# Kernel optimization log

Hardware: AMD Instinct MI355X
Metric: run time of the kernel (lower is better)

## Reference

```python
import jax, jax.numpy as jnp
import numpy as np

B, T, D, H = 8, 256, 1024, 512
NUM_SPANS = T * (T + 1) // 2          # triangular span enumeration
K = int(2.0 * T)                      # pruning_ratio * num_tokens
NUM_GOLD = 10
NEG = -1e20                           # allennlp replace_masked_values fill

# static triangular (start, end) index tables: for start in range(T): for end in range(start, T)
_starts = np.repeat(np.arange(T), np.arange(T, 0, -1))
_ends = np.concatenate([np.arange(s, T) for s in range(T)])
START_IDX = jnp.asarray(_starts, dtype=jnp.int32)
END_IDX = jnp.asarray(_ends, dtype=jnp.int32)


def setup_inputs() -> dict:
    key = jax.random.key(0)
    ks = jax.random.split(key, 8)
    inputs = jax.random.normal(ks[0], (B, T, D), dtype=jnp.float32)
    input_mask = jnp.ones((B, T), dtype=jnp.int32)
    # gold spans with start <= end, all in range (sorted along last dim)
    answer_spans = jnp.sort(jax.random.randint(ks[1], (B, NUM_GOLD, 2), 0, T), axis=-1)
    sD = 1.0 / np.sqrt(D)
    sH = 1.0 / np.sqrt(H)
    W_start = jax.random.uniform(ks[2], (D, H), jnp.float32, -sD, sD)
    b_start = jax.random.uniform(ks[3], (H,), jnp.float32, -sD, sD)
    W_end = jax.random.uniform(ks[4], (D, H), jnp.float32, -sD, sD)
    b_end = jax.random.uniform(ks[5], (H,), jnp.float32, -sD, sD)
    w_score = jax.random.uniform(ks[6], (H, 1), jnp.float32, -sH, sH)
    b_score = jax.random.uniform(ks[7], (1,), jnp.float32, -sH, sH)
    return {"inputs": inputs, "input_mask": input_mask, "answer_spans": answer_spans,
            "W_start": W_start, "b_start": b_start, "W_end": W_end, "b_end": b_end,
            "w_score": w_score, "b_score": b_score}


def reference(inputs, input_mask, answer_spans, W_start, b_start, W_end, b_end, w_score, b_score):
    # SpanRepAssembly: project starts/ends, pairwise-sum over triangular spans
    hs = inputs @ W_start + b_start                        # [B,T,H]
    he = inputs @ W_end + b_end                            # [B,T,H]
    span_hidden = hs[:, START_IDX, :] + he[:, END_IDX, :]  # [B,S,H]
    m = input_mask.astype(bool)
    span_mask = m[:, START_IDX] & m[:, END_IDX]            # [B,S]

    # span scorer: ReLU -> Linear(H,1)
    scores = jax.nn.relu(span_hidden) @ w_score + b_score  # [B,S,1]
    scores = jnp.where(span_mask[..., None], scores, NEG)

    # Pruner: top-k by score, indices sorted ascending, gather
    _, top_idx = jax.lax.top_k(scores[..., 0], K)          # [B,K]
    top_idx = jnp.sort(top_idx, axis=1)
    top_logits = jnp.take_along_axis(scores, top_idx[..., None], axis=1)       # [B,K,1]
    top_mask = jnp.take_along_axis(span_mask, top_idx, axis=1)[..., None].astype(jnp.float32)
    top_probs = jax.nn.sigmoid(top_logits) * top_mask

    # gold prediction map (union policy): labels[b, tri_index(span)] = 1
    s0 = answer_spans[..., 0].astype(jnp.int32)
    e0 = answer_spans[..., 1].astype(jnp.int32)
    gmask = (s0 >= 0)
    arg_idx = (2 * s0 * T - s0 * s0 + s0) // 2 + (e0 - s0)
    arg_idx = jnp.where(gmask, arg_idx, 0)
    labels = jnp.zeros((B, NUM_SPANS), jnp.float32)
    labels = labels.at[jnp.arange(B)[:, None], arg_idx].max(gmask.astype(jnp.float32))
    pred = jnp.take_along_axis(labels[..., None], top_idx[..., None], axis=1)  # [B,K,1]

    # BCE-with-logits, weight=top_mask, reduction='sum' (stable form)
    l = top_logits
    bce = jnp.maximum(l, 0.0) - l * pred + jnp.log1p(jnp.exp(-jnp.abs(l)))
    loss = jnp.sum(top_mask * bce)
    return top_probs, loss
```

## Files before the change

### kernel.cpp

```cpp
#include <hip/hip_runtime.h>
#include <hip/hip_bf16.h>
#include <math.h>

#define BB 8
#define TT 256
#define DD 1024
#define HH 512
#define NSPANS 32896
#define KK 512
#define NEGV -1e20f
#define NCH 32
#define CHSZ 1028
#define NT32 36

typedef __attribute__((ext_vector_type(8))) short bf16x8;
typedef __attribute__((ext_vector_type(4))) float f32x4;

__device__ inline unsigned short f2bf(float f) {
    unsigned u = __float_as_uint(f);
    return (unsigned short)((u + 0x7FFFu + ((u >> 16) & 1u)) >> 16);
}
__device__ inline float bf2f(unsigned short u) {
    return __uint_as_float(((unsigned)u) << 16);
}
__device__ inline void split3(float v, unsigned short& a, unsigned short& b,
                              unsigned short& c) {
    a = f2bf(v);           float r  = v - bf2f(a);
    b = f2bf(r);           float r2 = r - bf2f(b);
    c = f2bf(r2);
}

__global__ __launch_bounds__(256) void prep(
    const float* __restrict__ X,
    const float* __restrict__ Ws, const float* __restrict__ We,
    unsigned short* __restrict__ x0, unsigned short* __restrict__ x1,
    unsigned short* __restrict__ x2, unsigned short* __restrict__ wt,
    unsigned* __restrict__ zp)
{
    const int blk = blockIdx.x;
    const int tid = threadIdx.x;

    if (blk < 2048) {
        const int i4 = blk * 256 + tid;
        const float4 v = ((const float4*)X)[i4];
        const float vv[4] = {v.x, v.y, v.z, v.w};
        ushort4 h0, h1, h2;
        unsigned short* p0 = (unsigned short*)&h0;
        unsigned short* p1 = (unsigned short*)&h1;
        unsigned short* p2 = (unsigned short*)&h2;
        #pragma unroll
        for (int j = 0; j < 4; ++j) split3(vv[j], p0[j], p1[j], p2[j]);
        ((ushort4*)x0)[i4] = h0;
        ((ushort4*)x1)[i4] = h1;
        ((ushort4*)x2)[i4] = h2;
    } else if (blk < 3072) {
        __shared__ float lt[32][33];
        const int blk2 = blk - 2048;
        const int z   = blk2 >> 9;
        const int rem = blk2 & 511;
        const int k0  = (rem >> 4) * 32;
        const int h0  = (rem & 15) * 32;

        const float* Wz = z ? We : Ws;
        {
            const int row = tid >> 3, c4 = tid & 7;
            const float4 v = *(const float4*)&Wz[(k0 + row) * HH + h0 + c4 * 4];
            lt[row][c4*4 + 0] = v.x;
            lt[row][c4*4 + 1] = v.y;
            lt[row][c4*4 + 2] = v.z;
            lt[row][c4*4 + 3] = v.w;
        }
        __syncthreads();
        {
            const int n = h0 + (tid >> 3), kq = tid & 7;
            ushort4 o0, o1, o2;
            unsigned short* q0 = (unsigned short*)&o0;
            unsigned short* q1 = (unsigned short*)&o1;
            unsigned short* q2 = (unsigned short*)&o2;
            #pragma unroll
            for (int u = 0; u < 4; ++u)
                split3(lt[kq*4 + u][tid >> 3], q0[u], q1[u], q2[u]);
            unsigned short* base = wt + (size_t)z * 3 * 524288;
            const int off = n * 1024 + k0 + kq * 4;
            *(ushort4*)&base[0 * 524288 + off] = o0;
            *(ushort4*)&base[1 * 524288 + off] = o1;
            *(ushort4*)&base[2 * 524288 + off] = o2;
        }
    } else {
        const int i = (blk - 3072) * 256 + tid;
        for (int k = i; k < 32777; k += 32 * 256) zp[k] = 0u;
    }
}

__global__ __launch_bounds__(256) void gemm_mfma(
    const unsigned short* __restrict__ xs,
    const unsigned short* __restrict__ wt,
    const float* __restrict__ bs, const float* __restrict__ be,
    float* __restrict__ hs, float* __restrict__ he)
{
    const int bid = blockIdx.x;
    const int lg  = ((bid & 7) << 6) + (bid >> 3);
    const int z   = lg >> 8;
    const int my  = (lg & 255) >> 3, nx = lg & 7;
    const int m0 = my * 64, n0 = nx * 64;

    const unsigned short* __restrict__ W = wt + (size_t)z * 3 * 524288;
    const float* __restrict__ bias = z ? be : bs;
    float* __restrict__ Y = z ? he : hs;

    __shared__ __align__(16) unsigned short la[3][64][72];
    __shared__ __align__(16) unsigned short lb[3][64][72];

    const int tid = threadIdx.x;
    const int wave = tid >> 6, lane = tid & 63;
    const int wm = (wave >> 1) * 32, wn = (wave & 1) * 32;

    f32x4 acc[2][2];
    #pragma unroll
    for (int i = 0; i < 2; ++i)
        #pragma unroll
        for (int j = 0; j < 2; ++j) acc[i][j] = (f32x4){0.f, 0.f, 0.f, 0.f};

    const int rA = lane & 15;
    const int kq = lane >> 4;

    for (int kt = 0; kt < 16; ++kt) {
        const int k0 = kt * 64;
        __syncthreads();
        #pragma unroll
        for (int sp = 0; sp < 3; ++sp) {
            #pragma unroll
            for (int it = 0; it < 2; ++it) {
                const int idx = it * 256 + tid;
                const int row = idx >> 3, c8 = idx & 7;
                *(int4*)&la[sp][row][c8 * 8] =
                    *(const int4*)&xs[(size_t)sp * 2097152 + (m0 + row) * 1024 + k0 + c8 * 8];
                *(int4*)&lb[sp][row][c8 * 8] =
                    *(const int4*)&W[(size_t)sp * 524288 + (n0 + row) * 1024 + k0 + c8 * 8];
            }
        }
        __syncthreads();

        #pragma unroll
        for (int s = 0; s < 2; ++s) {
            const int kl = s * 32 + kq * 8;
            bf16x8 af[3][2], bg[3][2];
            #pragma unroll
            for (int sp = 0; sp < 3; ++sp) {
                #pragma unroll
                for (int f = 0; f < 2; ++f) {
                    af[sp][f] = *(const bf16x8*)&la[sp][wm + f * 16 + rA][kl];
                    bg[sp][f] = *(const bf16x8*)&lb[sp][wn + f * 16 + rA][kl];
                }
            }
            #pragma unroll
            for (int fm = 0; fm < 2; ++fm)
                #pragma unroll
                for (int fn = 0; fn < 2; ++fn) {
                    acc[fm][fn] = __builtin_amdgcn_mfma_f32_16x16x32_bf16(
                        af[0][fm], bg[0][fn], acc[fm][fn], 0, 0, 0);
                    acc[fm][fn] = __builtin_amdgcn_mfma_f32_16x16x32_bf16(
                        af[0][fm], bg[1][fn], acc[fm][fn], 0, 0, 0);
                    acc[fm][fn] = __builtin_amdgcn_mfma_f32_16x16x32_bf16(
                        af[1][fm], bg[0][fn], acc[fm][fn], 0, 0, 0);
                    acc[fm][fn] = __builtin_amdgcn_mfma_f32_16x16x32_bf16(
                        af[1][fm], bg[1][fn], acc[fm][fn], 0, 0, 0);
                    acc[fm][fn] = __builtin_amdgcn_mfma_f32_16x16x32_bf16(
                        af[0][fm], bg[2][fn], acc[fm][fn], 0, 0, 0);
                    acc[fm][fn] = __builtin_amdgcn_mfma_f32_16x16x32_bf16(
                        af[2][fm], bg[0][fn], acc[fm][fn], 0, 0, 0);
                }
        }
    }

    const int col = lane & 15, rq = lane >> 4;
    #pragma unroll
    for (int fm = 0; fm < 2; ++fm)
        #pragma unroll
        for (int fn = 0; fn < 2; ++fn) {
            const int nn = n0 + wn + fn * 16 + col;
            const float bv = bias[nn];
            #pragma unroll
            for (int r = 0; r < 4; ++r) {
                const int mm = m0 + wm + fm * 16 + rq * 4 + r;
                Y[mm * HH + nn] = acc[fm][fn][r] + bv;
            }
        }
}

__device__ inline unsigned f2key(float f) {
    unsigned u = __float_as_uint(f);
    return u ^ ((u & 0x80000000u) ? 0xFFFFFFFFu : 0x80000000u);
}

__global__ __launch_bounds__(256) void span_scores(
    const float* __restrict__ hs, const float* __restrict__ he,
    const float* __restrict__ w_score, const float* __restrict__ b_score,
    const int* __restrict__ input_mask, float* __restrict__ scores,
    unsigned* __restrict__ hist12)
{
    const int bx = blockIdx.x;
    const int b = bx / NT32;
    int tI = bx - b * NT32;
    int i = 0, cum = 0;
    while (tI >= cum + (8 - i)) { cum += 8 - i; ++i; }
    const int j = i + (tI - cum);
    const int s0 = i * 32, e0 = j * 32;

    __shared__ __align__(16) float shs[32][132];
    __shared__ __align__(16) float she[32][132];
    __shared__ __align__(16) float swc[128];
    __shared__ unsigned lh[2048];

    const int tid = threadIdx.x;
    const float4* hs4 = (const float4*)hs;
    const float4* he4 = (const float4*)he;

    for (int idx = tid; idx < 2048; idx += 256) lh[idx] = 0;

    const int ii = tid >> 4, jj = tid & 15;

    float4 acc[2][2];
    #pragma unroll
    for (int p = 0; p < 2; ++p)
        #pragma unroll
        for (int q = 0; q < 2; ++q) acc[p][q] = make_float4(0.f, 0.f, 0.f, 0.f);

    for (int ck = 0; ck < 4; ++ck) {
        const int kc = ck * 128;
        __syncthreads();
        #pragma unroll
        for (int l = 0; l < 4; ++l) {
            const int idx = l * 256 + tid;
            const int row = idx >> 5, c4 = idx & 31;
            *(float4*)&shs[row][c4 * 4] =
                hs4[((b*TT + s0 + row) * HH + kc) / 4 + c4];
            *(float4*)&she[row][c4 * 4] =
                he4[((b*TT + e0 + row) * HH + kc) / 4 + c4];
        }
        if (tid < 32) *(float4*)&swc[tid * 4] =
            ((const float4*)w_score)[kc / 4 + tid];
        __syncthreads();

        #pragma unroll 4
        for (int c4 = 0; c4 < 32; ++c4) {
            const float4 w  = *(const float4*)&swc[c4 * 4];
            const float4 a0 = *(const float4*)&shs[ii][c4 * 4];
            const float4 a1 = *(const float4*)&shs[ii + 16][c4 * 4];
            const float4 v0 = *(const float4*)&she[jj][c4 * 4];
            const float4 v1 = *(const float4*)&she[jj + 16][c4 * 4];
            #pragma unroll
            for (int p = 0; p < 2; ++p) {
                const float4 a = p ? a1 : a0;
                #pragma unroll
                for (int q = 0; q < 2; ++q) {
                    const float4 v = q ? v1 : v0;
                    acc[p][q].x += fmaxf(a.x + v.x, 0.f) * w.x;
                    acc[p][q].y += fmaxf(a.y + v.y, 0.f) * w.y;
                    acc[p][q].z += fmaxf(a.z + v.z, 0.f) * w.z;
                    acc[p][q].w += fmaxf(a.w + v.w, 0.f) * w.w;
                }
            }
        }
    }

    const float bsc = b_score[0];
    #pragma unroll
    for (int p = 0; p < 2; ++p) {
        const int s = s0 + ii + p * 16;
        #pragma unroll
        for (int q = 0; q < 2; ++q) {
            const int e = e0 + jj + q * 16;
            if (e >= s) {
                const float4 a4 = acc[p][q];
                float scv = (a4.x + a4.y) + (a4.z + a4.w) + bsc;
                if (!(input_mask[b*TT + s] && input_mask[b*TT + e])) scv = NEGV;
                scores[b*NSPANS + s*TT - (s*(s-1))/2 + (e - s)] = scv;
                const unsigned bin = f2key(scv) >> 20;
                atomicAdd(&lh[bin >> 1], 1u << ((bin & 1u) * 16));
            }
        }
    }
    __syncthreads();

    for (int idx = tid; idx < 2048; idx += 256) {
        const unsigned w = lh[idx];
        const unsigned lo = w & 0xFFFFu, hi = w >> 16;
        if (lo) atomicAdd(&hist12[b*4096 + 2*idx],     lo);
        if (hi) atomicAdd(&hist12[b*4096 + 2*idx + 1], hi);
    }
}

__global__ __launch_bounds__(256) void findcompact(
    const float* __restrict__ scores, const unsigned* __restrict__ hist12,
    unsigned* __restrict__ thrInfo,
    unsigned* __restrict__ cand, unsigned* __restrict__ candCnt)
{
    const int b = blockIdx.x >> 5, ch = blockIdx.x & 31;
    const unsigned* h = hist12 + b * 4096;
    const int tid = threadIdx.x;
    const int lane = tid & 63, wave = tid >> 6;

    const int topbin = 4095 - tid * 16;
    unsigned psum = 0;
    #pragma unroll
    for (int j = 0; j < 16; ++j) psum += h[topbin - j];

    unsigned inc = psum;
    #pragma unroll
    for (int off = 1; off < 64; off <<= 1) {
        unsigned v = __shfl_up(inc, off);
        if (lane >= off) inc += v;
    }
    __shared__ unsigned wsum4[4], wpre4[4];
    __shared__ unsigned shp[2];
    if (lane == 63) wsum4[wave] = inc;
    __syncthreads();
    if (tid == 0) { unsigned c = 0; for (int w = 0; w < 4; ++w) { wpre4[w] = c; c += wsum4[w]; } }
    __syncthreads();

    const unsigned before = wpre4[wave] + inc - psum;
    if (before < KK && before + psum >= KK) {
        unsigned cum = before;
        int bin = topbin;
        #pragma unroll
        for (int j = 0; j < 16; ++j) {
            const unsigned c = h[topbin - j];
            if (cum + c >= KK) { bin = topbin - j; break; }
            cum += c;
        }
        shp[0] = (unsigned)bin;
        shp[1] = KK - cum;
        thrInfo[b*4 + 0] = (unsigned)bin;
        thrInfo[b*4 + 1] = KK - cum;
    }
    __syncthreads();
    const unsigned p12 = shp[0];

    const float* sc = scores + b * NSPANS;
    const int base = ch * CHSZ;
    for (int i = base + tid; i < base + CHSZ; i += 256) {
        const unsigned key = f2key(sc[i]);
        if ((key >> 20) == p12) {
            const unsigned pos = atomicAdd(&candCnt[b], 1u);
            cand[b*NSPANS + pos] = key & 0xFFFFFu;
        }
    }
}

__global__ __launch_bounds__(1024) void refine(
    const unsigned* __restrict__ cand, const unsigned* __restrict__ candCnt,
    const float* __restrict__ scores,
    unsigned* __restrict__ thrInfo, unsigned* __restrict__ chunkBase)
{
    const int b = blockIdx.x;
    const unsigned* cd = cand + b*NSPANS;
    const unsigned n = candCnt[b];
    const unsigned remaining = thrInfo[b*4 + 1];
    const int tid = threadIdx.x;
    const int lane = tid & 63, wave = tid >> 6;

    __shared__ unsigned hist[1024];
    __shared__ unsigned wsum[16], wpre[16];
    __shared__ unsigned sh[2], shT[2];

    hist[tid] = 0;
    __syncthreads();
    for (unsigned i = tid; i < n; i += 1024) atomicAdd(&hist[(cd[i] >> 10) & 1023u], 1u);
    __syncthreads();
    {
        const unsigned psum = hist[1023 - tid];
        unsigned inc = psum;
        #pragma unroll
        for (int off = 1; off < 64; off <<= 1) {
            unsigned v = __shfl_up(inc, off);
            if (lane >= off) inc += v;
        }
        if (lane == 63) wsum[wave] = inc;
        __syncthreads();
        if (tid == 0) { unsigned c = 0; for (int w = 0; w < 16; ++w) { wpre[w] = c; c += wsum[w]; } }
        __syncthreads();
        const unsigned before = wpre[wave] + inc - psum;
        if (before < remaining && before + psum >= remaining && psum > 0) {
            sh[0] = 1023u - (unsigned)tid;
            sh[1] = remaining - before;
        }
        __syncthreads();
    }
    const unsigned b1 = sh[0], rem1 = sh[1];
    __syncthreads();

    hist[tid] = 0;
    __syncthreads();
    for (unsigned i = tid; i < n; i += 1024) {
        const unsigned v = cd[i];
        if (((v >> 10) & 1023u) == b1) atomicAdd(&hist[v & 1023u], 1u);
    }
    __syncthreads();
    {
        const unsigned psum = hist[1023 - tid];
        unsigned inc = psum;
        #pragma unroll
        for (int off = 1; off < 64; off <<= 1) {
            unsigned v = __shfl_up(inc, off);
            if (lane >= off) inc += v;
        }
        if (lane == 63) wsum[wave] = inc;
        __syncthreads();
        if (tid == 0) { unsigned c = 0; for (int w = 0; w < 16; ++w) { wpre[w] = c; c += wsum[w]; } }
        __syncthreads();
        const unsigned before = wpre[wave] + inc - psum;
        if (before < rem1 && before + psum >= rem1 && psum > 0) {
            const unsigned thrv = (thrInfo[b*4 + 0] << 20) | (b1 << 10) | (1023u - (unsigned)tid);
            thrInfo[b*4 + 2] = thrv;
            thrInfo[b*4 + 3] = rem1 - before;
            shT[0] = thrv;
            shT[1] = rem1 - before;
        }
    }
    __syncthreads();
    const unsigned thr = shT[0], ties = shT[1];

    __shared__ unsigned cg[NCH], ce[NCH];
    const float* sc = scores + b*NSPANS;
    #pragma unroll
    for (int q = 0; q < 2; ++q) {
        const int ch = wave*2 + q;
        const int base = ch*CHSZ, end = base + CHSZ;
        unsigned g = 0, e = 0;
        for (int i = base + lane; i < end; i += 64) {
            const unsigned key = f2key(sc[i]);
            g += (key > thr); e += (key == thr);
        }
        #pragma unroll
        for (int off = 32; off; off >>= 1) { g += __shfl_down(g, off); e += __shfl_down(e, off); }
        if (lane == 0) { cg[ch] = g; ce[ch] = e; }
    }
    __syncthreads();

    if (tid == 0) {
        unsigned out = 0, eqp = 0;
        for (int c = 0; c < NCH; ++c) {
            chunkBase[(b*NCH + c)*2 + 0] = out;
            chunkBase[(b*NCH + c)*2 + 1] = eqp;
            const unsigned room = (eqp >= ties) ? 0u : (ties - eqp);
            const unsigned taken = (ce[c] < room) ? ce[c] : room;
            out += cg[c] + taken;
            eqp += ce[c];
        }
    }
}

__global__ __launch_bounds__(256) void scatter_final(
    const float* __restrict__ scores, const unsigned* __restrict__ thrInfo,
    const unsigned* __restrict__ chunkBase, const int* __restrict__ answer_spans,
    float* __restrict__ chunkLoss, unsigned* __restrict__ ticket,
    float* __restrict__ out)
{
    const int b = blockIdx.x >> 5, ch = blockIdx.x & 31;
    const float* sc = scores + b*NSPANS;
    const unsigned thr = thrInfo[b*4 + 2], ties = thrInfo[b*4 + 3];
    unsigned outPos = chunkBase[(b*NCH + ch)*2 + 0];
    unsigned eqPos  = chunkBase[(b*NCH + ch)*2 + 1];

    const int tid = threadIdx.x, wave = tid >> 6, lane = tid & 63;
    const unsigned long long lmask = (1ull << lane) - 1ull;
    __shared__ unsigned wS[4], wE[4];
    __shared__ int gold[10];
    __shared__ float wLoss[4];
    __shared__ unsigned lastFlag;

    if (tid < 10) {
        const int s0 = answer_spans[b*20 + tid*2];
        const int e0 = answer_spans[b*20 + tid*2 + 1];
        gold[tid] = (s0 >= 0) ? ((2*s0*TT - s0*s0 + s0)/2 + (e0 - s0)) : -1;
    }
    __syncthreads();

    float lsum = 0.f;
    const int base = ch*CHSZ;
    for (int seg = base; seg < base + CHSZ; seg += 256) {
        const int i = seg + tid;
        const bool valid = (i < base + CHSZ);
        const float v = valid ? sc[i] : 0.f;
        const unsigned key = valid ? f2key(v) : 0u;
        const bool g  = valid && key > thr;
        const bool eq = valid && key == thr;

        const unsigned long long meq = __ballot(eq);
        if (lane == 0) wE[wave] = (unsigned)__popcll(meq);
        __syncthreads();

        unsigned eqPre = eqPos;
        for (int w = 0; w < wave; ++w) eqPre += wE[w];
        const unsigned myEqRank = eqPre + (unsigned)__popcll(meq & lmask);
        const bool sel = g || (eq && myEqRank < ties);

        const unsigned long long msel = __ballot(sel);
        if (lane == 0) wS[wave] = (unsigned)__popcll(msel);
        __syncthreads();

        unsigned selPre = outPos;
        for (int w = 0; w < wave; ++w) selPre += wS[w];
        if (sel) {
            const unsigned pos = b*KK + selPre + (unsigned)__popcll(msel & lmask);
            float prob = 0.f;
            if (v > -1e19f) {
                prob = 1.f / (1.f + expf(-v));
                float pred = 0.f;
                #pragma unroll
                for (int gq = 0; gq < 10; ++gq)
                    if (gold[gq] == i) pred = 1.f;
                lsum += fmaxf(v, 0.f) - v*pred + log1pf(expf(-fabsf(v)));
            }
            out[pos] = prob;
        }

        unsigned totS = 0, totE = 0;
        #pragma unroll
        for (int w = 0; w < 4; ++w) { totS += wS[w]; totE += wE[w]; }
        __syncthreads();
        outPos += totS; eqPos += totE;
    }

    #pragma unroll
    for (int off = 32; off; off >>= 1) lsum += __shfl_down(lsum, off);
    if (lane == 0) wLoss[wave] = lsum;
    __syncthreads();
    if (tid == 0) {
        chunkLoss[b*NCH + ch] = (wLoss[0] + wLoss[1]) + (wLoss[2] + wLoss[3]);
        __threadfence();
        lastFlag = atomicAdd(ticket, 1u);
    }
    __syncthreads();

    if (lastFlag == BB*NCH - 1) {
        __threadfence();
        float cl = atomicAdd(&chunkLoss[tid], 0.f);
        #pragma unroll
        for (int off = 32; off; off >>= 1) cl += __shfl_down(cl, off);
        if (lane == 0) wLoss[wave] = cl;
        __syncthreads();
        if (tid == 0)
            out[BB*KK] = (wLoss[0] + wLoss[1]) + (wLoss[2] + wLoss[3]);
    }
}

extern "C" void kernel_launch(void* const* d_in, const int* in_sizes, int n_in,
                              void* d_out, int out_size, void* d_ws, size_t ws_size,
                              hipStream_t stream)
{
    const float* inputs       = (const float*)d_in[0];
    const int*   input_mask   = (const int*)  d_in[1];
    const int*   answer_spans = (const int*)  d_in[2];
    const float* W_start      = (const float*)d_in[3];
    const float* b_start      = (const float*)d_in[4];
    const float* W_end        = (const float*)d_in[5];
    const float* b_end        = (const float*)d_in[6];
    const float* w_score      = (const float*)d_in[7];
    const float* b_score      = (const float*)d_in[8];
    float* out = (float*)d_out;
    unsigned* ws = (unsigned*)d_ws;

    float*    hs       = (float*)(ws);
    float*    he       = (float*)(ws + 1048576);
    float*    scores   = (float*)(ws + 2097152);
    unsigned* thrInfo  = ws + 2364416;
    unsigned* chunkBase= ws + 2364448;
    unsigned* hist12   = ws + 2364960;
    unsigned* candCnt  = ws + 2397728;
    unsigned* ticket   = ws + 2397736;
    unsigned short* xs = (unsigned short*)(ws + 2397740);
    unsigned short* wt = (unsigned short*)(ws + 5543468);
    float*    chunkLoss= (float*)(ws + 7116332);
    unsigned* cand     = (unsigned*)hs;

    prep<<<3104, 256, 0, stream>>>(inputs, W_start, W_end,
                                   xs, xs + 2097152, xs + 4194304, wt, hist12);

    gemm_mfma<<<512, 256, 0, stream>>>(xs, wt, b_start, b_end, hs, he);

    span_scores<<<BB*NT32, 256, 0, stream>>>(hs, he, w_score, b_score, input_mask,
                                             scores, hist12);

    findcompact  <<<BB*NCH, 256, 0, stream>>>(scores, hist12, thrInfo, cand, candCnt);
    refine       <<<BB, 1024, 0, stream>>>(cand, candCnt, scores, thrInfo, chunkBase);
    scatter_final<<<BB*NCH, 256, 0, stream>>>(scores, thrInfo, chunkBase,
                                              answer_spans, chunkLoss, ticket, out);
}
```

Baseline: 111.8 us.

## Fuse candidate compaction and threshold refinement via last-block ticket

```diff
diff --git a/kernel.cpp b/kernel.cpp
--- a/kernel.cpp
+++ b/kernel.cpp
@@ -88,7 +88,7 @@
         }
     } else {
         const int i = (blk - 3072) * 256 + tid;
-        for (int k = i; k < 32777; k += 32 * 256) zp[k] = 0u;
+        for (int k = i; k < 32785; k += 32 * 256) zp[k] = 0u;
     }
 }
 
@@ -291,142 +291,168 @@
     }
 }
 
-__global__ __launch_bounds__(256) void findcompact(
+__global__ __launch_bounds__(256) void findcompact_refine(
     const float* __restrict__ scores, const unsigned* __restrict__ hist12,
     unsigned* __restrict__ thrInfo,
-    unsigned* __restrict__ cand, unsigned* __restrict__ candCnt)
+    unsigned* __restrict__ cand, unsigned* __restrict__ candCnt,
+    unsigned* __restrict__ ticket2, unsigned* __restrict__ chunkBase)
 {
     const int b = blockIdx.x >> 5, ch = blockIdx.x & 31;
     const unsigned* h = hist12 + b * 4096;
     const int tid = threadIdx.x;
     const int lane = tid & 63, wave = tid >> 6;
 
-    const int topbin = 4095 - tid * 16;
-    unsigned psum = 0;
-    #pragma unroll
-    for (int j = 0; j < 16; ++j) psum += h[topbin - j];
-
-    unsigned inc = psum;
-    #pragma unroll
-    for (int off = 1; off < 64; off <<= 1) {
-        unsigned v = __shfl_up(inc, off);
-        if (lane >= off) inc += v;
-    }
     __shared__ unsigned wsum4[4], wpre4[4];
     __shared__ unsigned shp[2];
-    if (lane == 63) wsum4[wave] = inc;
-    __syncthreads();
-    if (tid == 0) { unsigned c = 0; for (int w = 0; w < 4; ++w) { wpre4[w] = c; c += wsum4[w]; } }
-    __syncthreads();
-
-    const unsigned before = wpre4[wave] + inc - psum;
-    if (before < KK && before + psum >= KK) {
-        unsigned cum = before;
-        int bin = topbin;
-        #pragma unroll
-        for (int j = 0; j < 16; ++j) {
-            const unsigned c = h[topbin - j];
-            if (cum + c >= KK) { bin = topbin - j; break; }
-            cum += c;
-        }
-        shp[0] = (unsigned)bin;
-        shp[1] = KK - cum;
-        thrInfo[b*4 + 0] = (unsigned)bin;
-        thrInfo[b*4 + 1] = KK - cum;
-    }
-    __syncthreads();
-    const unsigned p12 = shp[0];
-
-    const float* sc = scores + b * NSPANS;
-    const int base = ch * CHSZ;
-    for (int i = base + tid; i < base + CHSZ; i += 256) {
-        const unsigned key = f2key(sc[i]);
-        if ((key >> 20) == p12) {
-            const unsigned pos = atomicAdd(&candCnt[b], 1u);
-            cand[b*NSPANS + pos] = key & 0xFFFFFu;
-        }
-    }
-}
-
-__global__ __launch_bounds__(1024) void refine(
-    const unsigned* __restrict__ cand, const unsigned* __restrict__ candCnt,
-    const float* __restrict__ scores,
-    unsigned* __restrict__ thrInfo, unsigned* __restrict__ chunkBase)
-{
-    const int b = blockIdx.x;
-    const unsigned* cd = cand + b*NSPANS;
-    const unsigned n = candCnt[b];
-    const unsigned remaining = thrInfo[b*4 + 1];
-    const int tid = threadIdx.x;
-    const int lane = tid & 63, wave = tid >> 6;
-
+    __shared__ unsigned myTicket;
     __shared__ unsigned hist[1024];
-    __shared__ unsigned wsum[16], wpre[16];
-    __shared__ unsigned sh[2], shT[2];
-
-    hist[tid] = 0;
-    __syncthreads();
-    for (unsigned i = tid; i < n; i += 1024) atomicAdd(&hist[(cd[i] >> 10) & 1023u], 1u);
-    __syncthreads();
+    __shared__ unsigned shR[2];
+    __shared__ unsigned cg[NCH], ce[NCH];
+
     {
-        const unsigned psum = hist[1023 - tid];
+        const int topbin = 4095 - tid * 16;
+        unsigned psum = 0;
+        #pragma unroll
+        for (int j = 0; j < 16; ++j) psum += h[topbin - j];
+
         unsigned inc = psum;
         #pragma unroll
         for (int off = 1; off < 64; off <<= 1) {
             unsigned v = __shfl_up(inc, off);
             if (lane >= off) inc += v;
         }
-        if (lane == 63) wsum[wave] = inc;
-        __syncthreads();
-        if (tid == 0) { unsigned c = 0; for (int w = 0; w < 16; ++w) { wpre[w] = c; c += wsum[w]; } }
-        __syncthreads();
-        const unsigned before = wpre[wave] + inc - psum;
-        if (before < remaining && before + psum >= remaining && psum > 0) {
-            sh[0] = 1023u - (unsigned)tid;
-            sh[1] = remaining - before;
-        }
-        __syncthreads();
-    }
-    const unsigned b1 = sh[0], rem1 = sh[1];
-    __syncthreads();
-
-    hist[tid] = 0;
-    __syncthreads();
-    for (unsigned i = tid; i < n; i += 1024) {
-        const unsigned v = cd[i];
-        if (((v >> 10) & 1023u) == b1) atomicAdd(&hist[v & 1023u], 1u);
-    }
-    __syncthreads();
+        if (lane == 63) wsum4[wave] = inc;
+        __syncthreads();
+        if (tid == 0) { unsigned c = 0; for (int w = 0; w < 4; ++w) { wpre4[w] = c; c += wsum4[w]; } }
+        __syncthreads();
+
+        const unsigned before = wpre4[wave] + inc - psum;
+        if (before < KK && before + psum >= KK) {
+            unsigned cum = before;
+            int bin = topbin;
+            #pragma unroll
+            for (int j = 0; j < 16; ++j) {
+                const unsigned c = h[topbin - j];
+                if (cum + c >= KK) { bin = topbin - j; break; }
+                cum += c;
+            }
+            shp[0] = (unsigned)bin;
+            shp[1] = KK - cum;
+            thrInfo[b*4 + 0] = (unsigned)bin;
+            thrInfo[b*4 + 1] = KK - cum;
+        }
+    }
+    __syncthreads();
+    const unsigned p12 = shp[0];
+    const unsigned remaining = shp[1];
+
+    const float* sc = scores + b * NSPANS;
     {
-        const unsigned psum = hist[1023 - tid];
+        const int base = ch * CHSZ;
+        for (int i = base + tid; i < base + CHSZ; i += 256) {
+            const unsigned key = f2key(sc[i]);
+            if ((key >> 20) == p12) {
+                const unsigned pos = atomicAdd(&candCnt[b], 1u);
+                cand[b*NSPANS + pos] = key & 0xFFFFFu;
+            }
+        }
+    }
+    __syncthreads();
+    if (tid == 0) {
+        __threadfence();
+        myTicket = atomicAdd(&ticket2[b], 1u);
+    }
+    __syncthreads();
+    if (myTicket != NCH - 1) return;
+
+    __threadfence();
+    const unsigned n = atomicAdd(&candCnt[b], 0u);
+    unsigned* cd = cand + b * NSPANS;
+
+    for (int i = tid; i < 1024; i += 256) hist[i] = 0;
+    __syncthreads();
+    for (unsigned i = tid; i < n; i += 256) {
+        const unsigned v = atomicAdd(&cd[i], 0u);
+        atomicAdd(&hist[(v >> 10) & 1023u], 1u);
+    }
+    __syncthreads();
+    unsigned b1, rem1;
+    {
+        const int topbin = 1023 - tid * 4;
+        const unsigned psum = hist[topbin] + hist[topbin-1] + hist[topbin-2] + hist[topbin-3];
         unsigned inc = psum;
         #pragma unroll
         for (int off = 1; off < 64; off <<= 1) {
             unsigned v = __shfl_up(inc, off);
             if (lane >= off) inc += v;
         }
-        if (lane == 63) wsum[wave] = inc;
-        __syncthreads();
-        if (tid == 0) { unsigned c = 0; for (int w = 0; w < 16; ++w) { wpre[w] = c; c += wsum[w]; } }
-        __syncthreads();
-        const unsigned before = wpre[wave] + inc - psum;
+        if (lane == 63) wsum4[wave] = inc;
+        __syncthreads();
+        if (tid == 0) { unsigned c = 0; for (int w = 0; w < 4; ++w) { wpre4[w] = c; c += wsum4[w]; } }
+        __syncthreads();
+        const unsigned before = wpre4[wave] + inc - psum;
+        if (before < remaining && before + psum >= remaining && psum > 0) {
+            unsigned cum = before;
+            int bin = topbin;
+            #pragma unroll
+            for (int j = 0; j < 4; ++j) {
+                const unsigned c = hist[topbin - j];
+                if (cum + c >= remaining) { bin = topbin - j; break; }
+                cum += c;
+            }
+            shR[0] = (unsigned)bin;
+            shR[1] = remaining - cum;
+        }
+        __syncthreads();
+        b1 = shR[0]; rem1 = shR[1];
+    }
+    __syncthreads();
+
+    for (int i = tid; i < 1024; i += 256) hist[i] = 0;
+    __syncthreads();
+    for (unsigned i = tid; i < n; i += 256) {
+        const unsigned v = atomicAdd(&cd[i], 0u);
+        if (((v >> 10) & 1023u) == b1) atomicAdd(&hist[v & 1023u], 1u);
+    }
+    __syncthreads();
+    unsigned thr, ties;
+    {
+        const int topbin = 1023 - tid * 4;
+        const unsigned psum = hist[topbin] + hist[topbin-1] + hist[topbin-2] + hist[topbin-3];
+        unsigned inc = psum;
+        #pragma unroll
+        for (int off = 1; off < 64; off <<= 1) {
+            unsigned v = __shfl_up(inc, off);
+            if (lane >= off) inc += v;
+        }
+        if (lane == 63) wsum4[wave] = inc;
+        __syncthreads();
+        if (tid == 0) { unsigned c = 0; for (int w = 0; w < 4; ++w) { wpre4[w] = c; c += wsum4[w]; } }
+        __syncthreads();
+        const unsigned before = wpre4[wave] + inc - psum;
         if (before < rem1 && before + psum >= rem1 && psum > 0) {
-            const unsigned thrv = (thrInfo[b*4 + 0] << 20) | (b1 << 10) | (1023u - (unsigned)tid);
+            unsigned cum = before;
+            int bin = topbin;
+            #pragma unroll
+            for (int j = 0; j < 4; ++j) {
+                const unsigned c = hist[topbin - j];
+                if (cum + c >= rem1) { bin = topbin - j; break; }
+                cum += c;
+            }
+            const unsigned thrv = (p12 << 20) | (b1 << 10) | (unsigned)bin;
             thrInfo[b*4 + 2] = thrv;
-            thrInfo[b*4 + 3] = rem1 - before;
-            shT[0] = thrv;
-            shT[1] = rem1 - before;
-        }
-    }
-    __syncthreads();
-    const unsigned thr = shT[0], ties = shT[1];
-
-    __shared__ unsigned cg[NCH], ce[NCH];
-    const float* sc = scores + b*NSPANS;
-    #pragma unroll
-    for (int q = 0; q < 2; ++q) {
-        const int ch = wave*2 + q;
-        const int base = ch*CHSZ, end = base + CHSZ;
+            thrInfo[b*4 + 3] = rem1 - cum;
+            shR[0] = thrv;
+            shR[1] = rem1 - cum;
+        }
+        __syncthreads();
+        thr = shR[0]; ties = shR[1];
+    }
+    __syncthreads();
+
+    for (int q = 0; q < 8; ++q) {
+        const int ch2 = wave * 8 + q;
+        const int base = ch2 * CHSZ, end = base + CHSZ;
         unsigned g = 0, e = 0;
         for (int i = base + lane; i < end; i += 64) {
             const unsigned key = f2key(sc[i]);
@@ -434,7 +460,7 @@
         }
         #pragma unroll
         for (int off = 32; off; off >>= 1) { g += __shfl_down(g, off); e += __shfl_down(e, off); }
-        if (lane == 0) { cg[ch] = g; ce[ch] = e; }
+        if (lane == 0) { cg[ch2] = g; ce[ch2] = e; }
     }
     __syncthreads();
 
@@ -570,9 +596,10 @@
     unsigned* hist12   = ws + 2364960;
     unsigned* candCnt  = ws + 2397728;
     unsigned* ticket   = ws + 2397736;
-    unsigned short* xs = (unsigned short*)(ws + 2397740);
-    unsigned short* wt = (unsigned short*)(ws + 5543468);
-    float*    chunkLoss= (float*)(ws + 7116332);
+    unsigned* ticket2  = ws + 2397737;
+    unsigned short* xs = (unsigned short*)(ws + 2397748);
+    unsigned short* wt = (unsigned short*)(ws + 5543476);
+    float*    chunkLoss= (float*)(ws + 7116340);
     unsigned* cand     = (unsigned*)hs;
 
     prep<<<3104, 256, 0, stream>>>(inputs, W_start, W_end,
@@ -583,8 +610,9 @@
     span_scores<<<BB*NT32, 256, 0, stream>>>(hs, he, w_score, b_score, input_mask,
                                              scores, hist12);
 
-    findcompact  <<<BB*NCH, 256, 0, stream>>>(scores, hist12, thrInfo, cand, candCnt);
-    refine       <<<BB, 1024, 0, stream>>>(cand, candCnt, scores, thrInfo, chunkBase);
+    findcompact_refine<<<BB*NCH, 256, 0, stream>>>(scores, hist12, thrInfo,
+                                                   cand, candCnt, ticket2, chunkBase);
+
     scatter_final<<<BB*NCH, 256, 0, stream>>>(scores, thrInfo, chunkBase,
                                               answer_spans, chunkLoss, ticket, out);
 }
```

New measurement: 133.4 us. 19.4% more time.
